# Optimization experiments

Hardware: AMD Instinct MI355X
Metric: run time of the kernel (lower is better)

The kernel has to match this reference:

```python
import jax, jax.numpy as jnp
import numpy as np

B, N, E, H = 2, 2048, 512, 8
D = E // H
SCALE_BASE = 512.0
EPS = 1e-6


def _xpos_tables(n, d):
    # XPOS (torchscale): per-dim scale ramp + standard sinusoidal freqs
    half = d // 2
    xscale = (np.arange(0, d, 2, dtype=np.float32) + 0.4 * d) / (1.4 * d)  # [half]
    min_pos = -(n // 2)
    power = (np.arange(min_pos, n + min_pos, dtype=np.float32) / SCALE_BASE)[:, None]
    scale = xscale[None, :] ** power                                       # [n, half]
    inv_freq = 1.0 / (10000.0 ** (np.arange(0, half, dtype=np.float32) / half))
    sinusoid = np.arange(n, dtype=np.float32)[:, None] * inv_freq[None, :]  # [n, half]
    return (jnp.asarray(np.sin(sinusoid), jnp.float32),
            jnp.asarray(np.cos(sinusoid), jnp.float32),
            jnp.asarray(scale, jnp.float32))


def _dup_interleave(m):
    # [n, half] -> [n, d], each column repeated twice interleaved
    return jnp.repeat(m, 2, axis=-1)


def _rotate_every_two(x):
    x1, x2 = x[..., ::2], x[..., 1::2]
    return jnp.stack((-x2, x1), axis=-1).reshape(x.shape)


def _apply_xpos(x, sin, cos, scale):
    s = _dup_interleave(sin * scale)  # [n, d]
    c = _dup_interleave(cos * scale)
    return x * c + _rotate_every_two(x) * s


def _decay_mask(n, dtype=jnp.float32):
    # gammas per head: 1 - exp(linspace(log(1/32), log(1/512), H))
    gammas = 1.0 - jnp.exp(jnp.linspace(np.log(1.0 / 32), np.log(1.0 / 512), H)).astype(dtype)
    pos = jnp.arange(n, dtype=dtype)
    dist = pos[:, None] - pos[None, :]                 # [n, s]
    dist_c = jnp.where(dist >= 0, dist, 0.0)
    return jnp.where(dist[None] >= 0, gammas[:, None, None] ** dist_c[None], 0.0)  # [h, n, s]


def _msr_forward(query, key, value, Wq, bq, Wk, bk, Wv, bv, Wg, bg, Wo, bo):
    b, n, e = query.shape
    q = (query @ Wq.T + bq).reshape(b, n, H, D).transpose(0, 2, 1, 3)  # [b,h,n,d]
    k = (key   @ Wk.T + bk).reshape(b, n, H, D).transpose(0, 2, 1, 3)
    v = (value @ Wv.T + bv).reshape(b, n, H, D).transpose(0, 2, 1, 3)

    sin, cos, scale = _xpos_tables(n, D)
    q = _apply_xpos(q, sin, cos, scale)
    k = _apply_xpos(k, sin, cos, 1.0 / scale)  # downscale=True

    k = k / jnp.asarray(np.sqrt(D), q.dtype)   # scale = head_dim ** 0.5
    mask = _decay_mask(n, q.dtype)             # [h,n,s]

    sim = jnp.einsum('bhnd,bhsd->bhns', q, k) * mask[None]
    ret = jnp.einsum('bhns,bhsd->bhnd', sim, v)  # [b,h,n,d]

    # GroupNorm(groups=H, channels=H, affine=False) on [(b n), h, d]:
    # normalize each (b, n, h) slice over its d elements
    mean = ret.mean(axis=-1, keepdims=True)
    var = ret.var(axis=-1, keepdims=True)
    ret = (ret - mean) / jnp.sqrt(var + EPS)

    ret = ret.transpose(0, 2, 1, 3).reshape(b, n, e)
    gate = jax.nn.silu(query @ Wg.T + bg)
    return (ret * gate) @ Wo.T + bo


def setup_inputs() -> dict:
    key = jax.random.key(0)
    ks = jax.random.split(key, 13)
    std = float(np.sqrt(2.0 / (E + E)))  # xavier_normal for square Linear
    mk = lambda k: jax.random.normal(k, (E, E), jnp.float32) * std
    return {
        'query': jax.random.normal(ks[0], (B, N, E), jnp.float32),
        'key':   jax.random.normal(ks[1], (B, N, E), jnp.float32),
        'value': jax.random.normal(ks[2], (B, N, E), jnp.float32),
        'Wq': mk(ks[3]), 'bq': jnp.zeros((E,), jnp.float32),
        'Wk': mk(ks[4]), 'bk': jnp.zeros((E,), jnp.float32),
        'Wv': mk(ks[5]), 'bv': jnp.zeros((E,), jnp.float32),
        'Wg': mk(ks[6]), 'bg': jnp.zeros((E,), jnp.float32),
        'Wo': mk(ks[7]), 'bo': jnp.zeros((E,), jnp.float32),
    }


def reference(query, key, value, Wq, bq, Wk, bk, Wv, bv, Wg, bg, Wo, bo):
    return _msr_forward(query, key, value, Wq, bq, Wk, bk, Wv, bv, Wg, bg, Wo, bo)
```

## Files before the change

### kernel.cpp

```cpp
#include <hip/hip_runtime.h>
#include <math.h>

#define Bc 2
#define Nc 2048
#define Ec 512
#define Hc 8
#define Dc 64
#define Mc 4096
#define NT 32
#define Cc 64

typedef short bf16x8 __attribute__((ext_vector_type(8)));
typedef float f32x4 __attribute__((ext_vector_type(4)));

#define GLOAD(g, l) __builtin_amdgcn_global_load_lds(                        \
    (const __attribute__((address_space(1))) unsigned*)(const void*)(g),     \
    (__attribute__((address_space(3))) unsigned*)(void*)(l), 16, 0, 0)

#define VMCNT(n) asm volatile("s_waitcnt vmcnt(" #n ")" ::: "memory")

__device__ __forceinline__ unsigned short f2bf(float x) {
    union { float f; unsigned u; } v; v.f = x;
    unsigned r = v.u + 0x7fffu + ((v.u >> 16) & 1u);
    return (unsigned short)(r >> 16);
}
__device__ __forceinline__ float bf2f(unsigned short b) {
    union { float f; unsigned u; } v; v.u = ((unsigned)b) << 16;
    return v.f;
}

__device__ __forceinline__ float get_gamma(int h) {
    const float l0 = -3.4657359028f;
    const float l1 = -6.2383246250f;
    return 1.0f - expf(l0 + (l1 - l0) * ((float)h / 7.0f));
}

struct SplitArgs {
    const float* src[8];
    unsigned short* hi[8];
    unsigned short* lo[8];
    int n[8];
};

__global__ __launch_bounds__(256) void prep_kernel(SplitArgs a,
                                                   float* __restrict__ sinS,
                                                   float* __restrict__ cosS,
                                                   float* __restrict__ sinIS,
                                                   float* __restrict__ cosIS) {
    int y = blockIdx.y;
    if (y == 8) {
        int idx = blockIdx.x * 256 + threadIdx.x;
        if (idx >= Nc * 32) return;
        int n = idx & 2047;
        int i = idx >> 11;
        float xscale = (2.0f * (float)i + 25.6f) / 89.6f;
        float power  = ((float)n - 1024.0f) / 512.0f;
        float scale  = powf(xscale, power);
        float inv_freq = powf(10000.0f, -(float)i / 32.0f);
        float ang = (float)n * inv_freq;
        float s = sinf(ang), c = cosf(ang);
        int o = i * 2048 + n;
        sinS[o]  = s * scale;
        cosS[o]  = c * scale;
        float rs = 0.125f / scale;
        sinIS[o] = s * rs;
        cosIS[o] = c * rs;
        return;
    }
    int i4 = (blockIdx.x * 256 + threadIdx.x) * 4;
    if (i4 >= a.n[y]) return;
    float4 v = *(const float4*)&a.src[y][i4];
    ushort4 h, l;
    h.x = f2bf(v.x); l.x = f2bf(v.x - bf2f(h.x));
    h.y = f2bf(v.y); l.y = f2bf(v.y - bf2f(h.y));
    h.z = f2bf(v.z); l.z = f2bf(v.z - bf2f(h.z));
    h.w = f2bf(v.w); l.w = f2bf(v.w - bf2f(h.w));
    *(ushort4*)&a.hi[y][i4] = h;
    *(ushort4*)&a.lo[y][i4] = l;
}

template<int TM, int TN, int WR, int WC>
__global__ __launch_bounds__(WR * WC * 64) void mgemm_kernel(
    const unsigned short* __restrict__ Xq_h, const unsigned short* __restrict__ Xq_l,
    const unsigned short* __restrict__ Xk_h, const unsigned short* __restrict__ Xk_l,
    const unsigned short* __restrict__ Xv_h, const unsigned short* __restrict__ Xv_l,
    const unsigned short* __restrict__ Xr_h, const unsigned short* __restrict__ Xr_l,
    const unsigned short* __restrict__ Wq_h, const unsigned short* __restrict__ Wq_l,
    const unsigned short* __restrict__ Wk_h, const unsigned short* __restrict__ Wk_l,
    const unsigned short* __restrict__ Wv_h, const unsigned short* __restrict__ Wv_l,
    const unsigned short* __restrict__ Wg_h, const unsigned short* __restrict__ Wg_l,
    const unsigned short* __restrict__ Wo_h, const unsigned short* __restrict__ Wo_l,
    const float* __restrict__ bq, const float* __restrict__ bk, const float* __restrict__ bv,
    const float* __restrict__ bg, const float* __restrict__ bo,
    float* __restrict__ Qr, float* __restrict__ Kr, float* __restrict__ Vr,
    float* __restrict__ G, float* __restrict__ Out,
    const float* __restrict__ sinS, const float* __restrict__ cosS,
    const float* __restrict__ sinIS, const float* __restrict__ cosIS,
    int mode_base)
{
    constexpr int THREADS = WR * WC * 64;
    constexpr int MI  = TM / WR / 16;
    constexpr int NI  = TN / WC / 16;
    constexpr int RA  = TM * 4 / THREADS;
    constexpr int RB  = TN * 4 / THREADS;
    constexpr int GL  = 2 * (RA + RB);
    constexpr int BUF = (TM + TN) * 64;
    constexpr int ALo = TM * 32;
    constexpr int BHo = TM * 64;
    constexpr int BLo = TM * 64 + TN * 32;
    static_assert(GL == 6 || GL == 8, "vmcnt literal");

    int gx = gridDim.x, gy = gridDim.y;
    int nwg = gx * gy * gridDim.z;
    int id = blockIdx.x + gx * (blockIdx.y + gy * blockIdx.z);
    int sid = (id & 7) * (nwg >> 3) + (id >> 3);
    int bx = sid % gx; int rest = sid / gx;
    int by = rest % gy; int bz = rest / gy;

    int mode = mode_base + bz;
    const unsigned short *Xh, *Xl, *Wh, *Wl; const float* bias;
    switch (mode) {
        case 0:  Xh = Xq_h; Xl = Xq_l; Wh = Wq_h; Wl = Wq_l; bias = bq; break;
        case 1:  Xh = Xk_h; Xl = Xk_l; Wh = Wk_h; Wl = Wk_l; bias = bk; break;
        case 2:  Xh = Xv_h; Xl = Xv_l; Wh = Wv_h; Wl = Wv_l; bias = bv; break;
        case 3:  Xh = Xq_h; Xl = Xq_l; Wh = Wg_h; Wl = Wg_l; bias = bg; break;
        default: Xh = Xr_h; Xl = Xr_l; Wh = Wo_h; Wl = Wo_l; bias = bo; break;
    }

    __shared__ __align__(16) short lds[2 * BUF];

    int tid  = threadIdx.x;
    int lane = tid & 63;
    int w    = tid >> 6;
    int wr   = w / WC, wc = w % WC;
    int row0 = bx * TM, col0 = by * TN;
    int lrow = lane & 15, lslot = lane >> 4;

    f32x4 acc[MI][NI];
    #pragma unroll
    for (int i = 0; i < MI; ++i)
        #pragma unroll
        for (int j = 0; j < NI; ++j) acc[i][j] = {0.f, 0.f, 0.f, 0.f};

    int aoff[MI], boff[NI];
    #pragma unroll
    for (int mi = 0; mi < MI; ++mi) {
        int r = wr * (TM / WR) + mi * 16 + lrow;
        aoff[mi] = (r * 4 + (lslot ^ ((r >> 1) & 3))) * 8;
    }
    #pragma unroll
    for (int ni = 0; ni < NI; ++ni) {
        int r = wc * (TN / WC) + ni * 16 + lrow;
        boff[ni] = (r * 4 + (lslot ^ ((r >> 1) & 3))) * 8;
    }

    auto stage = [&](int buf, int k0) {
        short* l = &lds[buf * BUF];
        #pragma unroll
        for (int i = 0; i < RA; ++i) {
            int q = i * THREADS + tid;
            int r = q >> 2;
            int sp = (q & 3) ^ ((r >> 1) & 3);
            int base = (i * THREADS + (w << 6)) * 8;
            size_t ga = (size_t)(row0 + r) * Ec + k0 + sp * 8;
            GLOAD(Xh + ga, &l[base]);
            GLOAD(Xl + ga, &l[ALo + base]);
        }
        #pragma unroll
        for (int i = 0; i < RB; ++i) {
            int q = i * THREADS + tid;
            int r = q >> 2;
            int sp = (q & 3) ^ ((r >> 1) & 3);
            int base = (i * THREADS + (w << 6)) * 8;
            size_t gb = (size_t)(col0 + r) * Ec + k0 + sp * 8;
            GLOAD(Wh + gb, &l[BHo + base]);
            GLOAD(Wl + gb, &l[BLo + base]);
        }
    };

    stage(0, 0);
    for (int t = 0; t < Ec / 32; ++t) {
        int cur = t & 1;
        if (t < Ec / 32 - 1) {
            stage(cur ^ 1, (t + 1) * 32);
            if constexpr (GL == 6) VMCNT(6); else VMCNT(8);
        } else {
            VMCNT(0);
        }
        __builtin_amdgcn_s_barrier();
        __builtin_amdgcn_sched_barrier(0);

        const short* l = &lds[cur * BUF];
        bf16x8 ah[MI], al[MI], bh[NI], bl[NI];
        #pragma unroll
        for (int mi = 0; mi < MI; ++mi) {
            ah[mi] = *(const bf16x8*)&l[aoff[mi]];
            al[mi] = *(const bf16x8*)&l[ALo + aoff[mi]];
        }
        #pragma unroll
        for (int ni = 0; ni < NI; ++ni) {
            bh[ni] = *(const bf16x8*)&l[BHo + boff[ni]];
            bl[ni] = *(const bf16x8*)&l[BLo + boff[ni]];
        }
        #pragma unroll
        for (int mi = 0; mi < MI; ++mi)
            #pragma unroll
            for (int ni = 0; ni < NI; ++ni) {
                acc[mi][ni] = __builtin_amdgcn_mfma_f32_16x16x32_bf16(ah[mi], bh[ni], acc[mi][ni], 0, 0, 0);
                acc[mi][ni] = __builtin_amdgcn_mfma_f32_16x16x32_bf16(ah[mi], bl[ni], acc[mi][ni], 0, 0, 0);
                acc[mi][ni] = __builtin_amdgcn_mfma_f32_16x16x32_bf16(al[mi], bh[ni], acc[mi][ni], 0, 0, 0);
            }
        asm volatile("s_waitcnt lgkmcnt(0)" ::: "memory");
        __builtin_amdgcn_sched_barrier(0);
        __builtin_amdgcn_s_barrier();
    }

    int quad = lslot;
    if (mode <= 1) {
        const float* st = (mode == 0) ? sinS : sinIS;
        const float* ct = (mode == 0) ? cosS : cosIS;
        float* dst = (mode == 0) ? Qr : Kr;
        #pragma unroll
        for (int ni = 0; ni < NI; ++ni) {
            int c = col0 + wc * (TN / WC) + ni * 16 + lrow;
            int h = c >> 6, d = c & 63, pr = d >> 1;
            float bi = bias[c];
            #pragma unroll
            for (int mi = 0; mi < MI; ++mi) {
                int R0 = row0 + wr * (TM / WR) + mi * 16 + quad * 4;
                int bb = R0 >> 11;
                int n0 = R0 & 2047;
                float4 sv4 = *(const float4*)&st[pr * 2048 + n0];
                float4 cv4 = *(const float4*)&ct[pr * 2048 + n0];
                float svv[4] = {sv4.x, sv4.y, sv4.z, sv4.w};
                float cvv[4] = {cv4.x, cv4.y, cv4.z, cv4.w};
                #pragma unroll
                for (int reg = 0; reg < 4; ++reg) {
                    float x = acc[mi][ni][reg] + bi;
                    float p = __shfl_xor(x, 1, 64);
                    float y = (c & 1) ? fmaf(x, cvv[reg],  p * svv[reg])
                                      : fmaf(x, cvv[reg], -p * svv[reg]);
                    dst[(((size_t)(bb * Hc + h)) * Nc + n0 + reg) * Dc + d] = y;
                }
            }
        }
    } else if (mode == 2) {
        #pragma unroll
        for (int ni = 0; ni < NI; ++ni) {
            int c = col0 + wc * (TN / WC) + ni * 16 + lrow;
            int h = c >> 6, d = c & 63;
            float bi = bias[c];
            #pragma unroll
            for (int mi = 0; mi < MI; ++mi) {
                int R0 = row0 + wr * (TM / WR) + mi * 16 + quad * 4;
                int bb = R0 >> 11;
                int n0 = R0 & 2047;
                #pragma unroll
                for (int reg = 0; reg < 4; ++reg)
                    Vr[(((size_t)(bb * Hc + h)) * Nc + n0 + reg) * Dc + d] =
                        acc[mi][ni][reg] + bi;
            }
        }
    } else {
        #pragma unroll
        for (int ni = 0; ni < NI; ++ni) {
            int c = col0 + wc * (TN / WC) + ni * 16 + lrow;
            float bi = bias[c];
            #pragma unroll
            for (int mi = 0; mi < MI; ++mi) {
                int R0 = row0 + wr * (TM / WR) + mi * 16 + quad * 4;
                #pragma unroll
                for (int reg = 0; reg < 4; ++reg) {
                    float x = acc[mi][ni][reg] + bi;
                    if (mode == 3)
                        G[(size_t)(R0 + reg) * Ec + c] = x / (1.0f + expf(-x));
                    else
                        Out[(size_t)(R0 + reg) * Ec + c] = x;
                }
            }
        }
    }
}

__global__ __launch_bounds__(256) void phaseA_kernel(const float* __restrict__ Kr,
                                                     const float* __restrict__ Vr,
                                                     float* __restrict__ L)
{
    int bh = blockIdx.x;
    int t  = blockIdx.y;
    float gamma = get_gamma(bh & 7);
    float lg = logf(gamma);

    __shared__ float Ks[64][68];
    __shared__ float Vs[64][68];

    int tid = threadIdx.x;
    const float* Kc = Kr + (size_t)(bh * Nc + t * Cc) * Dc;
    const float* Vc = Vr + (size_t)(bh * Nc + t * Cc) * Dc;

    #pragma unroll
    for (int i = 0; i < 4; ++i) {
        int f = tid + i * 256;
        int s = f >> 4;
        int d = (f & 15) << 2;
        float w = expf(lg * (float)(Cc - s));
        float4 kv = *(const float4*)&Kc[s * Dc + d];
        float4 ks = {kv.x * w, kv.y * w, kv.z * w, kv.w * w};
        *(float4*)&Ks[s][d] = ks;
        float4 vv = *(const float4*)&Vc[s * Dc + d];
        *(float4*)&Vs[s][d] = vv;
    }
    __syncthreads();

    int tx = tid & 15, ty = tid >> 4;
    float acc[4][4];
    #pragma unroll
    for (int i = 0; i < 4; ++i)
        #pragma unroll
        for (int j = 0; j < 4; ++j) acc[i][j] = 0.0f;

    for (int s = 0; s < 64; ++s) {
        float4 a = *(const float4*)&Ks[s][ty * 4];
        float4 b = *(const float4*)&Vs[s][tx * 4];
        float av[4] = {a.x, a.y, a.z, a.w};
        float bv[4] = {b.x, b.y, b.z, b.w};
        #pragma unroll
        for (int i = 0; i < 4; ++i)
            #pragma unroll
            for (int j = 0; j < 4; ++j)
                acc[i][j] = fmaf(av[i], bv[j], acc[i][j]);
    }

    float* Lp = L + (size_t)(bh * NT + t) * 4096;
    #pragma unroll
    for (int i = 0; i < 4; ++i) {
        float4 o = {acc[i][0], acc[i][1], acc[i][2], acc[i][3]};
        *(float4*)&Lp[(ty * 4 + i) * 64 + tx * 4] = o;
    }
}

__global__ __launch_bounds__(256) void scan_kernel(const float* __restrict__ L,
                                                   float* __restrict__ Sst)
{
    int bh = blockIdx.x;
    int part = blockIdx.y;
    int tid = threadIdx.x;
    float gamma = get_gamma(bh & 7);
    float g64 = expf(logf(gamma) * 64.0f);

    float4 s = {0.0f, 0.0f, 0.0f, 0.0f};
    size_t base = (size_t)bh * NT * 4096 + part * 1024 + tid * 4;
    const float* Lp = L + base;
    float* Sp = Sst + base;
    for (int t = 0; t < NT; ++t) {
        *(float4*)&Sp[(size_t)t * 4096] = s;
        float4 l = *(const float4*)&Lp[(size_t)t * 4096];
        s.x = s.x * g64 + l.x;
        s.y = s.y * g64 + l.y;
        s.z = s.z * g64 + l.z;
        s.w = s.w * g64 + l.w;
    }
}

__global__ __launch_bounds__(256) void phaseC_kernel(
    const float* __restrict__ Qr, const float* __restrict__ Kr, const float* __restrict__ Vr,
    const float* __restrict__ Sst, const float* __restrict__ G,
    unsigned short* __restrict__ retGh, unsigned short* __restrict__ retGl)
{
    int bh = blockIdx.x, t = blockIdx.y;
    int b = bh >> 3, h = bh & 7;
    float gamma = get_gamma(h);
    float lg = logf(gamma);

    __shared__ float QsT[64][68];
    __shared__ float KsT[64][68];
    __shared__ float Ss[64][68];

    int tid = threadIdx.x;
    const float* Qc = Qr + (size_t)(bh * Nc + t * Cc) * Dc;
    const float* Kc = Kr + (size_t)(bh * Nc + t * Cc) * Dc;
    const float* Sp = Sst + (size_t)(bh * NT + t) * 4096;

    #pragma unroll
    for (int i = 0; i < 4; ++i) {
        int f = tid + i * 256;
        int r = f >> 4;
        int d = (f & 15) << 2;
        float wq = expf(lg * (float)r);
        float4 q = *(const float4*)&Qc[r * Dc + d];
        QsT[d + 0][r] = q.x * wq; QsT[d + 1][r] = q.y * wq;
        QsT[d + 2][r] = q.z * wq; QsT[d + 3][r] = q.w * wq;
        float wk = expf(-lg * (float)r);
        float4 kk = *(const float4*)&Kc[r * Dc + d];
        KsT[d + 0][r] = kk.x * wk; KsT[d + 1][r] = kk.y * wk;
        KsT[d + 2][r] = kk.z * wk; KsT[d + 3][r] = kk.w * wk;
        float4 sv = *(const float4*)&Sp[r * 64 + d];
        *(float4*)&Ss[r][d] = sv;
    }
    __syncthreads();

    int tx = tid & 15, ty = tid >> 4;
    float accA[4][4], accO[4][4];
    #pragma unroll
    for (int i = 0; i < 4; ++i)
        #pragma unroll
        for (int j = 0; j < 4; ++j) { accA[i][j] = 0.0f; accO[i][j] = 0.0f; }

    for (int d = 0; d < 64; ++d) {
        float4 a  = *(const float4*)&QsT[d][ty * 4];
        float4 kb = *(const float4*)&KsT[d][tx * 4];
        float4 sb = *(const float4*)&Ss[d][tx * 4];
        float av[4] = {a.x, a.y, a.z, a.w};
        float kv[4] = {kb.x, kb.y, kb.z, kb.w};
        float sv[4] = {sb.x, sb.y, sb.z, sb.w};
        #pragma unroll
        for (int i = 0; i < 4; ++i)
            #pragma unroll
            for (int j = 0; j < 4; ++j) {
                accA[i][j] = fmaf(av[i], kv[j], accA[i][j]);
                accO[i][j] = fmaf(av[i], sv[j], accO[i][j]);
            }
    }
    __syncthreads();

    #pragma unroll
    for (int i = 0; i < 4; ++i) {
        int gi = ty * 4 + i;
        #pragma unroll
        for (int j = 0; j < 4; ++j) {
            int gj = tx * 4 + j;
            KsT[gj][gi] = (gj <= gi) ? accA[i][j] : 0.0f;
        }
    }
    const float* Vc = Vr + (size_t)(bh * Nc + t * Cc) * Dc;
    #pragma unroll
    for (int i = 0; i < 4; ++i) {
        int f = tid + i * 256;
        int r = f >> 4;
        int d = (f & 15) << 2;
        float4 vv = *(const float4*)&Vc[r * Dc + d];
        *(float4*)&QsT[r][d] = vv;
    }
    __syncthreads();

    for (int j = 0; j < 64; ++j) {
        float4 a = *(const float4*)&KsT[j][ty * 4];
        float4 v = *(const float4*)&QsT[j][tx * 4];
        float av[4] = {a.x, a.y, a.z, a.w};
        float vv[4] = {v.x, v.y, v.z, v.w};
        #pragma unroll
        for (int i = 0; i < 4; ++i)
            #pragma unroll
            for (int jj = 0; jj < 4; ++jj)
                accO[i][jj] = fmaf(av[i], vv[jj], accO[i][jj]);
    }

    #pragma unroll
    for (int i = 0; i < 4; ++i) {
        float sum = accO[i][0] + accO[i][1] + accO[i][2] + accO[i][3];
        float sq  = accO[i][0] * accO[i][0] + accO[i][1] * accO[i][1]
                  + accO[i][2] * accO[i][2] + accO[i][3] * accO[i][3];
        #pragma unroll
        for (int m = 1; m < 16; m <<= 1) {
            sum += __shfl_xor(sum, m, 64);
            sq  += __shfl_xor(sq,  m, 64);
        }
        float mean = sum * (1.0f / 64.0f);
        float var  = sq * (1.0f / 64.0f) - mean * mean;
        float rinv = rsqrtf(var + 1e-6f);
        #pragma unroll
        for (int jj = 0; jj < 4; ++jj)
            accO[i][jj] = (accO[i][jj] - mean) * rinv;
    }

    #pragma unroll
    for (int i = 0; i < 4; ++i) {
        int n = t * Cc + ty * 4 + i;
        size_t idx = ((size_t)b * Nc + n) * Ec + h * Dc + tx * 4;
        float4 g = *(const float4*)&G[idx];
        float o0 = accO[i][0] * g.x, o1 = accO[i][1] * g.y;
        float o2 = accO[i][2] * g.z, o3 = accO[i][3] * g.w;
        ushort4 hh, ll;
        hh.x = f2bf(o0); ll.x = f2bf(o0 - bf2f(hh.x));
        hh.y = f2bf(o1); ll.y = f2bf(o1 - bf2f(hh.y));
        hh.z = f2bf(o2); ll.z = f2bf(o2 - bf2f(hh.z));
        hh.w = f2bf(o3); ll.w = f2bf(o3 - bf2f(hh.w));
        *(ushort4*)&retGh[idx] = hh;
        *(ushort4*)&retGl[idx] = ll;
    }
}

extern "C" void kernel_launch(void* const* d_in, const int* in_sizes, int n_in,
                              void* d_out, int out_size, void* d_ws, size_t ws_size,
                              hipStream_t stream) {
    const float* query = (const float*)d_in[0];
    const float* key   = (const float*)d_in[1];
    const float* value = (const float*)d_in[2];
    const float* Wq = (const float*)d_in[3];
    const float* bq = (const float*)d_in[4];
    const float* Wk = (const float*)d_in[5];
    const float* bk = (const float*)d_in[6];
    const float* Wv = (const float*)d_in[7];
    const float* bv = (const float*)d_in[8];
    const float* Wg = (const float*)d_in[9];
    const float* bg = (const float*)d_in[10];
    const float* Wo = (const float*)d_in[11];
    const float* bo = (const float*)d_in[12];
    float* out = (float*)d_out;

    float* wsf = (float*)d_ws;
    const size_t SZ = (size_t)Bc * Nc * Ec;

    float* Qr = wsf;
    float* Kr = Qr + SZ;
    float* Vr = Kr + SZ;
    float* G  = Vr + SZ;

    unsigned short* Xq_h = (unsigned short*)(wsf + 4 * SZ);
    unsigned short* Xq_l = Xq_h + SZ;
    unsigned short* Xk_h = Xq_l + SZ;
    unsigned short* Xk_l = Xk_h + SZ;
    unsigned short* Xv_h = Xk_l + SZ;
    unsigned short* Xv_l = Xv_h + SZ;
    float* L   = wsf + 4 * SZ;
    float* Sst = wsf + 5 * SZ;
    unsigned short* retGh = (unsigned short*)(wsf + 6 * SZ);
    unsigned short* retGl = retGh + SZ;

    const size_t WSZ = (size_t)Ec * Ec;
    unsigned short* Wp = (unsigned short*)(wsf + 7 * SZ);
    unsigned short* Wq_h = Wp;            unsigned short* Wq_l = Wp + WSZ;
    unsigned short* Wk_h = Wp + 2 * WSZ;  unsigned short* Wk_l = Wp + 3 * WSZ;
    unsigned short* Wv_h = Wp + 4 * WSZ;  unsigned short* Wv_l = Wp + 5 * WSZ;
    unsigned short* Wg_h = Wp + 6 * WSZ;  unsigned short* Wg_l = Wp + 7 * WSZ;
    unsigned short* Wo_h = Wp + 8 * WSZ;  unsigned short* Wo_l = Wp + 9 * WSZ;

    float* tab = wsf + 7 * SZ + (10 * WSZ) / 2;
    float* sinS  = tab;
    float* cosS  = sinS + Nc * 32;
    float* sinIS = cosS + Nc * 32;
    float* cosIS = sinIS + Nc * 32;

    SplitArgs sa;
    sa.src[0] = query; sa.hi[0] = Xq_h; sa.lo[0] = Xq_l; sa.n[0] = (int)SZ;
    sa.src[1] = key;   sa.hi[1] = Xk_h; sa.lo[1] = Xk_l; sa.n[1] = (int)SZ;
    sa.src[2] = value; sa.hi[2] = Xv_h; sa.lo[2] = Xv_l; sa.n[2] = (int)SZ;
    sa.src[3] = Wq;    sa.hi[3] = Wq_h; sa.lo[3] = Wq_l; sa.n[3] = (int)WSZ;
    sa.src[4] = Wk;    sa.hi[4] = Wk_h; sa.lo[4] = Wk_l; sa.n[4] = (int)WSZ;
    sa.src[5] = Wv;    sa.hi[5] = Wv_h; sa.lo[5] = Wv_l; sa.n[5] = (int)WSZ;
    sa.src[6] = Wg;    sa.hi[6] = Wg_h; sa.lo[6] = Wg_l; sa.n[6] = (int)WSZ;
    sa.src[7] = Wo;    sa.hi[7] = Wo_h; sa.lo[7] = Wo_l; sa.n[7] = (int)WSZ;
    prep_kernel<<<dim3(2048, 9), dim3(256), 0, stream>>>(sa, sinS, cosS, sinIS, cosIS);

    mgemm_kernel<128, 256, 2, 4><<<dim3(Mc / 128, Ec / 256, 4), dim3(512), 0, stream>>>(
        Xq_h, Xq_l, Xk_h, Xk_l, Xv_h, Xv_l, retGh, retGl,
        Wq_h, Wq_l, Wk_h, Wk_l, Wv_h, Wv_l, Wg_h, Wg_l, Wo_h, Wo_l,
        bq, bk, bv, bg, bo, Qr, Kr, Vr, G, out,
        sinS, cosS, sinIS, cosIS, 0);

    phaseA_kernel<<<dim3(Bc * Hc, NT), dim3(256), 0, stream>>>(Kr, Vr, L);
    scan_kernel<<<dim3(Bc * Hc, 4), dim3(256), 0, stream>>>(L, Sst);
    phaseC_kernel<<<dim3(Bc * Hc, NT), dim3(256), 0, stream>>>(Qr, Kr, Vr, Sst, G, retGh, retGl);

    mgemm_kernel<128, 128, 2, 2><<<dim3(Mc / 128, Ec / 128, 1), dim3(256), 0, stream>>>(
        Xq_h, Xq_l, Xk_h, Xk_l, Xv_h, Xv_l, retGh, retGl,
        Wq_h, Wq_l, Wk_h, Wk_l, Wv_h, Wv_l, Wg_h, Wg_l, Wo_h, Wo_l,
        bq, bk, bv, bg, bo, Qr, Kr, Vr, G, out,
        sinS, cosS, sinIS, cosIS, 4);
}
```

Measured before the change: 189.1 us.

## Triple-buffer GEMM with load portions interleaved between MFMA phases

The double-buffered GEMM main loop becomes a triple-buffered one that prefetches two K-steps ahead. Each step is split into four phases, one per B column block. Each phase issues a slice of the next global-to-LDS loads, then runs its MFMAs at raised wave priority. The output-projection GEMM also moves to 64x128 tiles to launch more workgroups. The aim is to hide memory latency behind MFMA work, at the cost of more LDS per block and more barriers per K-step.

```diff
diff --git a/kernel.cpp b/kernel.cpp
--- a/kernel.cpp
+++ b/kernel.cpp
@@ -103,12 +103,12 @@
     constexpr int NI  = TN / WC / 16;
     constexpr int RA  = TM * 4 / THREADS;
     constexpr int RB  = TN * 4 / THREADS;
-    constexpr int GL  = 2 * (RA + RB);
     constexpr int BUF = (TM + TN) * 64;
     constexpr int ALo = TM * 32;
     constexpr int BHo = TM * 64;
     constexpr int BLo = TM * 64 + TN * 32;
-    static_assert(GL == 6 || GL == 8, "vmcnt literal");
+    constexpr int NSTEP = Ec / 32;
+    static_assert(RA == 1 && RB == 2 && NI == 4, "phase schedule assumes this shape");
 
     int gx = gridDim.x, gy = gridDim.y;
     int nwg = gx * gy * gridDim.z;
@@ -127,7 +127,7 @@
         default: Xh = Xr_h; Xl = Xr_l; Wh = Wo_h; Wl = Wo_l; bias = bo; break;
     }
 
-    __shared__ __align__(16) short lds[2 * BUF];
+    __shared__ __align__(16) short lds[3 * BUF];
 
     int tid  = threadIdx.x;
     int lane = tid & 63;
@@ -154,14 +154,13 @@
         boff[ni] = (r * 4 + (lslot ^ ((r >> 1) & 3))) * 8;
     }
 
-    auto stage = [&](int buf, int k0) {
+    auto stage_full = [&](int buf, int k0) {
         short* l = &lds[buf * BUF];
-        #pragma unroll
-        for (int i = 0; i < RA; ++i) {
-            int q = i * THREADS + tid;
+        {
+            int q = tid;
             int r = q >> 2;
             int sp = (q & 3) ^ ((r >> 1) & 3);
-            int base = (i * THREADS + (w << 6)) * 8;
+            int base = (w << 6) * 8;
             size_t ga = (size_t)(row0 + r) * Ec + k0 + sp * 8;
             GLOAD(Xh + ga, &l[base]);
             GLOAD(Xl + ga, &l[ALo + base]);
@@ -177,42 +176,66 @@
             GLOAD(Wl + gb, &l[BLo + base]);
         }
     };
-
-    stage(0, 0);
-    for (int t = 0; t < Ec / 32; ++t) {
-        int cur = t & 1;
-        if (t < Ec / 32 - 1) {
-            stage(cur ^ 1, (t + 1) * 32);
-            if constexpr (GL == 6) VMCNT(6); else VMCNT(8);
-        } else {
-            VMCNT(0);
-        }
-        __builtin_amdgcn_s_barrier();
-        __builtin_amdgcn_sched_barrier(0);
-
+    auto stage_portion = [&](int buf, int k0, int p) {
+        short* l = &lds[buf * BUF];
+        if (p == 0) {
+            int q = tid;
+            int r = q >> 2;
+            int sp = (q & 3) ^ ((r >> 1) & 3);
+            int base = (w << 6) * 8;
+            size_t ga = (size_t)(row0 + r) * Ec + k0 + sp * 8;
+            GLOAD(Xh + ga, &l[base]);
+            GLOAD(Xl + ga, &l[ALo + base]);
+        } else if (p <= 2) {
+            int i = p - 1;
+            int q = i * THREADS + tid;
+            int r = q >> 2;
+            int sp = (q & 3) ^ ((r >> 1) & 3);
+            int base = (i * THREADS + (w << 6)) * 8;
+            size_t gb = (size_t)(col0 + r) * Ec + k0 + sp * 8;
+            GLOAD(Wh + gb, &l[BHo + base]);
+            GLOAD(Wl + gb, &l[BLo + base]);
+        }
+    };
+
+    stage_full(0, 0);
+    stage_full(1, 32);
+    VMCNT(6);
+    __builtin_amdgcn_s_barrier();
+
+    bf16x8 ah[MI], al[MI];
+    for (int t = 0; t < NSTEP; ++t) {
+        const int cur = t % 3;
         const short* l = &lds[cur * BUF];
-        bf16x8 ah[MI], al[MI], bh[NI], bl[NI];
-        #pragma unroll
-        for (int mi = 0; mi < MI; ++mi) {
-            ah[mi] = *(const bf16x8*)&l[aoff[mi]];
-            al[mi] = *(const bf16x8*)&l[ALo + aoff[mi]];
-        }
-        #pragma unroll
-        for (int ni = 0; ni < NI; ++ni) {
-            bh[ni] = *(const bf16x8*)&l[BHo + boff[ni]];
-            bl[ni] = *(const bf16x8*)&l[BLo + boff[ni]];
-        }
-        #pragma unroll
-        for (int mi = 0; mi < MI; ++mi)
-            #pragma unroll
-            for (int ni = 0; ni < NI; ++ni) {
-                acc[mi][ni] = __builtin_amdgcn_mfma_f32_16x16x32_bf16(ah[mi], bh[ni], acc[mi][ni], 0, 0, 0);
-                acc[mi][ni] = __builtin_amdgcn_mfma_f32_16x16x32_bf16(ah[mi], bl[ni], acc[mi][ni], 0, 0, 0);
-                acc[mi][ni] = __builtin_amdgcn_mfma_f32_16x16x32_bf16(al[mi], bh[ni], acc[mi][ni], 0, 0, 0);
+        const bool pre = (t + 2) < NSTEP;
+        const int nb = (t + 2) % 3;
+        const int nk = (t + 2) * 32;
+        #pragma unroll
+        for (int p = 0; p < 4; ++p) {
+            if (p == 0) {
+                #pragma unroll
+                for (int mi = 0; mi < MI; ++mi) {
+                    ah[mi] = *(const bf16x8*)&l[aoff[mi]];
+                    al[mi] = *(const bf16x8*)&l[ALo + aoff[mi]];
+                }
             }
-        asm volatile("s_waitcnt lgkmcnt(0)" ::: "memory");
-        __builtin_amdgcn_sched_barrier(0);
-        __builtin_amdgcn_s_barrier();
+            bf16x8 bh2 = *(const bf16x8*)&l[BHo + boff[p]];
+            bf16x8 bl2 = *(const bf16x8*)&l[BLo + boff[p]];
+            if (pre) stage_portion(nb, nk, p);
+            __builtin_amdgcn_s_barrier();
+            asm volatile("s_waitcnt lgkmcnt(0)" ::: "memory");
+            __builtin_amdgcn_sched_barrier(0);
+            __builtin_amdgcn_s_setprio(1);
+            #pragma unroll
+            for (int mi = 0; mi < MI; ++mi) {
+                acc[mi][p] = __builtin_amdgcn_mfma_f32_16x16x32_bf16(ah[mi], bh2, acc[mi][p], 0, 0, 0);
+                acc[mi][p] = __builtin_amdgcn_mfma_f32_16x16x32_bf16(ah[mi], bl2, acc[mi][p], 0, 0, 0);
+                acc[mi][p] = __builtin_amdgcn_mfma_f32_16x16x32_bf16(al[mi], bh2, acc[mi][p], 0, 0, 0);
+            }
+            __builtin_amdgcn_s_setprio(0);
+            if (p == 3) { if (pre) VMCNT(6); else VMCNT(0); }
+            __builtin_amdgcn_s_barrier();
+        }
     }
 
     int quad = lslot;
@@ -237,9 +260,9 @@
                 #pragma unroll
                 for (int reg = 0; reg < 4; ++reg) {
                     float x = acc[mi][ni][reg] + bi;
-                    float p = __shfl_xor(x, 1, 64);
-                    float y = (c & 1) ? fmaf(x, cvv[reg],  p * svv[reg])
-                                      : fmaf(x, cvv[reg], -p * svv[reg]);
+                    float p2 = __shfl_xor(x, 1, 64);
+                    float y = (c & 1) ? fmaf(x, cvv[reg],  p2 * svv[reg])
+                                      : fmaf(x, cvv[reg], -p2 * svv[reg]);
                     dst[(((size_t)(bb * Hc + h)) * Nc + n0 + reg) * Dc + d] = y;
                 }
             }
@@ -562,7 +585,7 @@
     scan_kernel<<<dim3(Bc * Hc, 4), dim3(256), 0, stream>>>(L, Sst);
     phaseC_kernel<<<dim3(Bc * Hc, NT), dim3(256), 0, stream>>>(Qr, Kr, Vr, Sst, G, retGh, retGl);
 
-    mgemm_kernel<128, 128, 2, 2><<<dim3(Mc / 128, Ec / 128, 1), dim3(256), 0, stream>>>(
+    mgemm_kernel<64, 128, 2, 2><<<dim3(Mc / 64, Ec / 128, 1), dim3(256), 0, stream>>>(
         Xq_h, Xq_l, Xk_h, Xk_l, Xv_h, Xv_l, retGh, retGl,
         Wq_h, Wq_l, Wk_h, Wk_l, Wv_h, Wv_l, Wg_h, Wg_l, Wo_h, Wo_l,
         bq, bk, bv, bg, bo, Qr, Kr, Vr, G, out,
```

Measured after the change: 178.1 us. 1.06x faster.

## Replace split-bf16 three-pass GEMMs with single fp16 MFMA and retune tiles

Applied to the files above, without the earlier changes.

Replaces the hi/lo bf16 split representation (three MFMAs per tile pair plus double loads) with a single fp16 conversion and one f16 MFMA per tile, halving staging traffic and cutting matrix work by about three times. The GEMM tile shapes are also changed (the QKVG projection uses 128x128 with 256 threads, the output projection uses 64x128), and the scan kernel is regridded to more, smaller blocks. The epilogue is moved into a helper. The main risk is accuracy: fp16 has a narrower range and fewer mantissa bits than the compensated split, so the result may drift from the fp32 reference.

```diff
diff --git a/kernel.cpp b/kernel.cpp
--- a/kernel.cpp
+++ b/kernel.cpp
@@ -10,7 +10,7 @@
 #define NT 32
 #define Cc 64
 
-typedef short bf16x8 __attribute__((ext_vector_type(8)));
+typedef _Float16 f16x8 __attribute__((ext_vector_type(8)));
 typedef float f32x4 __attribute__((ext_vector_type(4)));
 
 #define GLOAD(g, l) __builtin_amdgcn_global_load_lds(                        \
@@ -19,15 +19,7 @@
 
 #define VMCNT(n) asm volatile("s_waitcnt vmcnt(" #n ")" ::: "memory")
 
-__device__ __forceinline__ unsigned short f2bf(float x) {
-    union { float f; unsigned u; } v; v.f = x;
-    unsigned r = v.u + 0x7fffu + ((v.u >> 16) & 1u);
-    return (unsigned short)(r >> 16);
-}
-__device__ __forceinline__ float bf2f(unsigned short b) {
-    union { float f; unsigned u; } v; v.u = ((unsigned)b) << 16;
-    return v.f;
-}
+union H4 { _Float16 h[4]; ushort4 u; };
 
 __device__ __forceinline__ float get_gamma(int h) {
     const float l0 = -3.4657359028f;
@@ -37,8 +29,7 @@
 
 struct SplitArgs {
     const float* src[8];
-    unsigned short* hi[8];
-    unsigned short* lo[8];
+    unsigned short* dst[8];
     int n[8];
 };
 
@@ -70,26 +61,94 @@
     int i4 = (blockIdx.x * 256 + threadIdx.x) * 4;
     if (i4 >= a.n[y]) return;
     float4 v = *(const float4*)&a.src[y][i4];
-    ushort4 h, l;
-    h.x = f2bf(v.x); l.x = f2bf(v.x - bf2f(h.x));
-    h.y = f2bf(v.y); l.y = f2bf(v.y - bf2f(h.y));
-    h.z = f2bf(v.z); l.z = f2bf(v.z - bf2f(h.z));
-    h.w = f2bf(v.w); l.w = f2bf(v.w - bf2f(h.w));
-    *(ushort4*)&a.hi[y][i4] = h;
-    *(ushort4*)&a.lo[y][i4] = l;
+    H4 o;
+    o.h[0] = (_Float16)v.x; o.h[1] = (_Float16)v.y;
+    o.h[2] = (_Float16)v.z; o.h[3] = (_Float16)v.w;
+    *(ushort4*)&a.dst[y][i4] = o.u;
+}
+
+template<int TM, int TN, int WR, int WC, int MI, int NI>
+__device__ __forceinline__ void gemm_epilogue(
+    f32x4 (&acc)[MI][NI], int mode, int row0, int col0, int wr, int wc,
+    int lrow, int quad, const float* bias,
+    float* Qr, float* Kr, float* Vr, float* G, float* Out,
+    unsigned short* retG,
+    const float* sinS, const float* cosS,
+    const float* sinIS, const float* cosIS)
+{
+    if (mode <= 1) {
+        const float* st = (mode == 0) ? sinS : sinIS;
+        const float* ct = (mode == 0) ? cosS : cosIS;
+        float* dst = (mode == 0) ? Qr : Kr;
+        #pragma unroll
+        for (int ni = 0; ni < NI; ++ni) {
+            int c = col0 + wc * (TN / WC) + ni * 16 + lrow;
+            int h = c >> 6, d = c & 63, pr = d >> 1;
+            float bi = bias[c];
+            #pragma unroll
+            for (int mi = 0; mi < MI; ++mi) {
+                int R0 = row0 + wr * (TM / WR) + mi * 16 + quad * 4;
+                int bb = R0 >> 11;
+                int n0 = R0 & 2047;
+                float4 sv4 = *(const float4*)&st[pr * 2048 + n0];
+                float4 cv4 = *(const float4*)&ct[pr * 2048 + n0];
+                float svv[4] = {sv4.x, sv4.y, sv4.z, sv4.w};
+                float cvv[4] = {cv4.x, cv4.y, cv4.z, cv4.w};
+                #pragma unroll
+                for (int reg = 0; reg < 4; ++reg) {
+                    float x = acc[mi][ni][reg] + bi;
+                    float p2 = __shfl_xor(x, 1, 64);
+                    float y = (c & 1) ? fmaf(x, cvv[reg],  p2 * svv[reg])
+                                      : fmaf(x, cvv[reg], -p2 * svv[reg]);
+                    dst[(((size_t)(bb * Hc + h)) * Nc + n0 + reg) * Dc + d] = y;
+                }
+            }
+        }
+    } else if (mode == 2) {
+        #pragma unroll
+        for (int ni = 0; ni < NI; ++ni) {
+            int c = col0 + wc * (TN / WC) + ni * 16 + lrow;
+            int h = c >> 6, d = c & 63;
+            float bi = bias[c];
+            #pragma unroll
+            for (int mi = 0; mi < MI; ++mi) {
+                int R0 = row0 + wr * (TM / WR) + mi * 16 + quad * 4;
+                int bb = R0 >> 11;
+                int n0 = R0 & 2047;
+                #pragma unroll
+                for (int reg = 0; reg < 4; ++reg)
+                    Vr[(((size_t)(bb * Hc + h)) * Nc + n0 + reg) * Dc + d] =
+                        acc[mi][ni][reg] + bi;
+            }
+        }
+    } else {
+        #pragma unroll
+        for (int ni = 0; ni < NI; ++ni) {
+            int c = col0 + wc * (TN / WC) + ni * 16 + lrow;
+            float bi = bias[c];
+            #pragma unroll
+            for (int mi = 0; mi < MI; ++mi) {
+                int R0 = row0 + wr * (TM / WR) + mi * 16 + quad * 4;
+                #pragma unroll
+                for (int reg = 0; reg < 4; ++reg) {
+                    float x = acc[mi][ni][reg] + bi;
+                    if (mode == 3)
+                        G[(size_t)(R0 + reg) * Ec + c] = x / (1.0f + expf(-x));
+                    else
+                        Out[(size_t)(R0 + reg) * Ec + c] = x;
+                }
+            }
+        }
+    }
 }
 
 template<int TM, int TN, int WR, int WC>
 __global__ __launch_bounds__(WR * WC * 64) void mgemm_kernel(
-    const unsigned short* __restrict__ Xq_h, const unsigned short* __restrict__ Xq_l,
-    const unsigned short* __restrict__ Xk_h, const unsigned short* __restrict__ Xk_l,
-    const unsigned short* __restrict__ Xv_h, const unsigned short* __restrict__ Xv_l,
-    const unsigned short* __restrict__ Xr_h, const unsigned short* __restrict__ Xr_l,
-    const unsigned short* __restrict__ Wq_h, const unsigned short* __restrict__ Wq_l,
-    const unsigned short* __restrict__ Wk_h, const unsigned short* __restrict__ Wk_l,
-    const unsigned short* __restrict__ Wv_h, const unsigned short* __restrict__ Wv_l,
-    const unsigned short* __restrict__ Wg_h, const unsigned short* __restrict__ Wg_l,
-    const unsigned short* __restrict__ Wo_h, const unsigned short* __restrict__ Wo_l,
+    const unsigned short* __restrict__ Xq, const unsigned short* __restrict__ Xk,
+    const unsigned short* __restrict__ Xv, const unsigned short* __restrict__ Xr,
+    const unsigned short* __restrict__ Wq, const unsigned short* __restrict__ Wk,
+    const unsigned short* __restrict__ Wv, const unsigned short* __restrict__ Wg,
+    const unsigned short* __restrict__ Wo,
     const float* __restrict__ bq, const float* __restrict__ bk, const float* __restrict__ bv,
     const float* __restrict__ bg, const float* __restrict__ bo,
     float* __restrict__ Qr, float* __restrict__ Kr, float* __restrict__ Vr,
@@ -103,12 +162,10 @@
     constexpr int NI  = TN / WC / 16;
     constexpr int RA  = TM * 4 / THREADS;
     constexpr int RB  = TN * 4 / THREADS;
-    constexpr int GL  = 2 * (RA + RB);
-    constexpr int BUF = (TM + TN) * 64;
-    constexpr int ALo = TM * 32;
-    constexpr int BHo = TM * 64;
-    constexpr int BLo = TM * 64 + TN * 32;
-    static_assert(GL == 6 || GL == 8, "vmcnt literal");
+    constexpr int GL  = RA + RB;
+    constexpr int BUF = (TM + TN) * 32;
+    constexpr int BHo = TM * 32;
+    static_assert(GL == 3 || GL == 4, "vmcnt literal");
 
     int gx = gridDim.x, gy = gridDim.y;
     int nwg = gx * gy * gridDim.z;
@@ -118,16 +175,16 @@
     int by = rest % gy; int bz = rest / gy;
 
     int mode = mode_base + bz;
-    const unsigned short *Xh, *Xl, *Wh, *Wl; const float* bias;
+    const unsigned short *Xh, *Wh; const float* bias;
     switch (mode) {
-        case 0:  Xh = Xq_h; Xl = Xq_l; Wh = Wq_h; Wl = Wq_l; bias = bq; break;
-        case 1:  Xh = Xk_h; Xl = Xk_l; Wh = Wk_h; Wl = Wk_l; bias = bk; break;
-        case 2:  Xh = Xv_h; Xl = Xv_l; Wh = Wv_h; Wl = Wv_l; bias = bv; break;
-        case 3:  Xh = Xq_h; Xl = Xq_l; Wh = Wg_h; Wl = Wg_l; bias = bg; break;
-        default: Xh = Xr_h; Xl = Xr_l; Wh = Wo_h; Wl = Wo_l; bias = bo; break;
-    }
-
-    __shared__ __align__(16) short lds[2 * BUF];
+        case 0:  Xh = Xq; Wh = Wq; bias = bq; break;
+        case 1:  Xh = Xk; Wh = Wk; bias = bk; break;
+        case 2:  Xh = Xv; Wh = Wv; bias = bv; break;
+        case 3:  Xh = Xq; Wh = Wg; bias = bg; break;
+        default: Xh = Xr; Wh = Wo; bias = bo; break;
+    }
+
+    __shared__ __align__(16) unsigned short lds[2 * BUF];
 
     int tid  = threadIdx.x;
     int lane = tid & 63;
@@ -155,7 +212,7 @@
     }
 
     auto stage = [&](int buf, int k0) {
-        short* l = &lds[buf * BUF];
+        unsigned short* l = &lds[buf * BUF];
         #pragma unroll
         for (int i = 0; i < RA; ++i) {
             int q = i * THREADS + tid;
@@ -164,7 +221,6 @@
             int base = (i * THREADS + (w << 6)) * 8;
             size_t ga = (size_t)(row0 + r) * Ec + k0 + sp * 8;
             GLOAD(Xh + ga, &l[base]);
-            GLOAD(Xl + ga, &l[ALo + base]);
         }
         #pragma unroll
         for (int i = 0; i < RB; ++i) {
@@ -174,7 +230,6 @@
             int base = (i * THREADS + (w << 6)) * 8;
             size_t gb = (size_t)(col0 + r) * Ec + k0 + sp * 8;
             GLOAD(Wh + gb, &l[BHo + base]);
-            GLOAD(Wl + gb, &l[BLo + base]);
         }
     };
 
@@ -183,103 +238,34 @@
         int cur = t & 1;
         if (t < Ec / 32 - 1) {
             stage(cur ^ 1, (t + 1) * 32);
-            if constexpr (GL == 6) VMCNT(6); else VMCNT(8);
+            if constexpr (GL == 4) VMCNT(4); else VMCNT(3);
         } else {
             VMCNT(0);
         }
         __builtin_amdgcn_s_barrier();
         __builtin_amdgcn_sched_barrier(0);
 
-        const short* l = &lds[cur * BUF];
-        bf16x8 ah[MI], al[MI], bh[NI], bl[NI];
-        #pragma unroll
-        for (int mi = 0; mi < MI; ++mi) {
-            ah[mi] = *(const bf16x8*)&l[aoff[mi]];
-            al[mi] = *(const bf16x8*)&l[ALo + aoff[mi]];
-        }
-        #pragma unroll
-        for (int ni = 0; ni < NI; ++ni) {
-            bh[ni] = *(const bf16x8*)&l[BHo + boff[ni]];
-            bl[ni] = *(const bf16x8*)&l[BLo + boff[ni]];
-        }
+        const unsigned short* l = &lds[cur * BUF];
+        f16x8 ah[MI], bh[NI];
         #pragma unroll
         for (int mi = 0; mi < MI; ++mi)
-            #pragma unroll
-            for (int ni = 0; ni < NI; ++ni) {
-                acc[mi][ni] = __builtin_amdgcn_mfma_f32_16x16x32_bf16(ah[mi], bh[ni], acc[mi][ni], 0, 0, 0);
-                acc[mi][ni] = __builtin_amdgcn_mfma_f32_16x16x32_bf16(ah[mi], bl[ni], acc[mi][ni], 0, 0, 0);
-                acc[mi][ni] = __builtin_amdgcn_mfma_f32_16x16x32_bf16(al[mi], bh[ni], acc[mi][ni], 0, 0, 0);
-            }
+            ah[mi] = *(const f16x8*)&l[aoff[mi]];
+        #pragma unroll
+        for (int ni = 0; ni < NI; ++ni)
+            bh[ni] = *(const f16x8*)&l[BHo + boff[ni]];
+        #pragma unroll
+        for (int mi = 0; mi < MI; ++mi)
+            #pragma unroll
+            for (int ni = 0; ni < NI; ++ni)
+                acc[mi][ni] = __builtin_amdgcn_mfma_f32_16x16x32_f16(ah[mi], bh[ni], acc[mi][ni], 0, 0, 0);
         asm volatile("s_waitcnt lgkmcnt(0)" ::: "memory");
         __builtin_amdgcn_sched_barrier(0);
         __builtin_amdgcn_s_barrier();
     }
 
-    int quad = lslot;
-    if (mode <= 1) {
-        const float* st = (mode == 0) ? sinS : sinIS;
-        const float* ct = (mode == 0) ? cosS : cosIS;
-        float* dst = (mode == 0) ? Qr : Kr;
-        #pragma unroll
-        for (int ni = 0; ni < NI; ++ni) {
-            int c = col0 + wc * (TN / WC) + ni * 16 + lrow;
-            int h = c >> 6, d = c & 63, pr = d >> 1;
-            float bi = bias[c];
-            #pragma unroll
-            for (int mi = 0; mi < MI; ++mi) {
-                int R0 = row0 + wr * (TM / WR) + mi * 16 + quad * 4;
-                int bb = R0 >> 11;
-                int n0 = R0 & 2047;
-                float4 sv4 = *(const float4*)&st[pr * 2048 + n0];
-                float4 cv4 = *(const float4*)&ct[pr * 2048 + n0];
-                float svv[4] = {sv4.x, sv4.y, sv4.z, sv4.w};
-                float cvv[4] = {cv4.x, cv4.y, cv4.z, cv4.w};
-                #pragma unroll
-                for (int reg = 0; reg < 4; ++reg) {
-                    float x = acc[mi][ni][reg] + bi;
-                    float p = __shfl_xor(x, 1, 64);
-                    float y = (c & 1) ? fmaf(x, cvv[reg],  p * svv[reg])
-                                      : fmaf(x, cvv[reg], -p * svv[reg]);
-                    dst[(((size_t)(bb * Hc + h)) * Nc + n0 + reg) * Dc + d] = y;
-                }
-            }
-        }
-    } else if (mode == 2) {
-        #pragma unroll
-        for (int ni = 0; ni < NI; ++ni) {
-            int c = col0 + wc * (TN / WC) + ni * 16 + lrow;
-            int h = c >> 6, d = c & 63;
-            float bi = bias[c];
-            #pragma unroll
-            for (int mi = 0; mi < MI; ++mi) {
-                int R0 = row0 + wr * (TM / WR) + mi * 16 + quad * 4;
-                int bb = R0 >> 11;
-                int n0 = R0 & 2047;
-                #pragma unroll
-                for (int reg = 0; reg < 4; ++reg)
-                    Vr[(((size_t)(bb * Hc + h)) * Nc + n0 + reg) * Dc + d] =
-                        acc[mi][ni][reg] + bi;
-            }
-        }
-    } else {
-        #pragma unroll
-        for (int ni = 0; ni < NI; ++ni) {
-            int c = col0 + wc * (TN / WC) + ni * 16 + lrow;
-            float bi = bias[c];
-            #pragma unroll
-            for (int mi = 0; mi < MI; ++mi) {
-                int R0 = row0 + wr * (TM / WR) + mi * 16 + quad * 4;
-                #pragma unroll
-                for (int reg = 0; reg < 4; ++reg) {
-                    float x = acc[mi][ni][reg] + bi;
-                    if (mode == 3)
-                        G[(size_t)(R0 + reg) * Ec + c] = x / (1.0f + expf(-x));
-                    else
-                        Out[(size_t)(R0 + reg) * Ec + c] = x;
-                }
-            }
-        }
-    }
+    gemm_epilogue<TM, TN, WR, WC, MI, NI>(acc, mode, row0, col0, wr, wc,
+        lrow, lslot, bias, Qr, Kr, Vr, G, Out, (unsigned short*)nullptr,
+        sinS, cosS, sinIS, cosIS);
 }
 
 __global__ __launch_bounds__(256) void phaseA_kernel(const float* __restrict__ Kr,
@@ -339,8 +325,8 @@
     }
 }
 
-__global__ __launch_bounds__(256) void scan_kernel(const float* __restrict__ L,
-                                                   float* __restrict__ Sst)
+__global__ __launch_bounds__(64) void scan_kernel(const float* __restrict__ L,
+                                                  float* __restrict__ Sst)
 {
     int bh = blockIdx.x;
     int part = blockIdx.y;
@@ -349,7 +335,7 @@
     float g64 = expf(logf(gamma) * 64.0f);
 
     float4 s = {0.0f, 0.0f, 0.0f, 0.0f};
-    size_t base = (size_t)bh * NT * 4096 + part * 1024 + tid * 4;
+    size_t base = (size_t)bh * NT * 4096 + part * 256 + tid * 4;
     const float* Lp = L + base;
     float* Sp = Sst + base;
     for (int t = 0; t < NT; ++t) {
@@ -365,7 +351,7 @@
 __global__ __launch_bounds__(256) void phaseC_kernel(
     const float* __restrict__ Qr, const float* __restrict__ Kr, const float* __restrict__ Vr,
     const float* __restrict__ Sst, const float* __restrict__ G,
-    unsigned short* __restrict__ retGh, unsigned short* __restrict__ retGl)
+    unsigned short* __restrict__ retG)
 {
     int bh = blockIdx.x, t = blockIdx.y;
     int b = bh >> 3, h = bh & 7;
@@ -478,15 +464,12 @@
         int n = t * Cc + ty * 4 + i;
         size_t idx = ((size_t)b * Nc + n) * Ec + h * Dc + tx * 4;
         float4 g = *(const float4*)&G[idx];
-        float o0 = accO[i][0] * g.x, o1 = accO[i][1] * g.y;
-        float o2 = accO[i][2] * g.z, o3 = accO[i][3] * g.w;
-        ushort4 hh, ll;
-        hh.x = f2bf(o0); ll.x = f2bf(o0 - bf2f(hh.x));
-        hh.y = f2bf(o1); ll.y = f2bf(o1 - bf2f(hh.y));
-        hh.z = f2bf(o2); ll.z = f2bf(o2 - bf2f(hh.z));
-        hh.w = f2bf(o3); ll.w = f2bf(o3 - bf2f(hh.w));
-        *(ushort4*)&retGh[idx] = hh;
-        *(ushort4*)&retGl[idx] = ll;
+        H4 o;
+        o.h[0] = (_Float16)(accO[i][0] * g.x);
+        o.h[1] = (_Float16)(accO[i][1] * g.y);
+        o.h[2] = (_Float16)(accO[i][2] * g.z);
+        o.h[3] = (_Float16)(accO[i][3] * g.w);
+        *(ushort4*)&retG[idx] = o.u;
     }
 }
 
@@ -516,55 +499,52 @@
     float* Vr = Kr + SZ;
     float* G  = Vr + SZ;
 
-    unsigned short* Xq_h = (unsigned short*)(wsf + 4 * SZ);
-    unsigned short* Xq_l = Xq_h + SZ;
-    unsigned short* Xk_h = Xq_l + SZ;
-    unsigned short* Xk_l = Xk_h + SZ;
-    unsigned short* Xv_h = Xk_l + SZ;
-    unsigned short* Xv_l = Xv_h + SZ;
-    float* L   = wsf + 4 * SZ;
-    float* Sst = wsf + 5 * SZ;
-    unsigned short* retGh = (unsigned short*)(wsf + 6 * SZ);
-    unsigned short* retGl = retGh + SZ;
+    unsigned short* Xq_f  = (unsigned short*)(wsf + 4 * SZ);
+    unsigned short* Xk_f  = Xq_f + SZ;
+    unsigned short* Xv_f  = Xk_f + SZ;
+    unsigned short* retGf = Xv_f + SZ;
+
+    float* L   = wsf + 6 * SZ;
+    float* Sst = wsf + 7 * SZ;
 
     const size_t WSZ = (size_t)Ec * Ec;
-    unsigned short* Wp = (unsigned short*)(wsf + 7 * SZ);
-    unsigned short* Wq_h = Wp;            unsigned short* Wq_l = Wp + WSZ;
-    unsigned short* Wk_h = Wp + 2 * WSZ;  unsigned short* Wk_l = Wp + 3 * WSZ;
-    unsigned short* Wv_h = Wp + 4 * WSZ;  unsigned short* Wv_l = Wp + 5 * WSZ;
-    unsigned short* Wg_h = Wp + 6 * WSZ;  unsigned short* Wg_l = Wp + 7 * WSZ;
-    unsigned short* Wo_h = Wp + 8 * WSZ;  unsigned short* Wo_l = Wp + 9 * WSZ;
-
-    float* tab = wsf + 7 * SZ + (10 * WSZ) / 2;
+    unsigned short* Wp = (unsigned short*)(wsf + 8 * SZ);
+    unsigned short* Wq_f = Wp;
+    unsigned short* Wk_f = Wp + WSZ;
+    unsigned short* Wv_f = Wp + 2 * WSZ;
+    unsigned short* Wg_f = Wp + 3 * WSZ;
+    unsigned short* Wo_f = Wp + 4 * WSZ;
+
+    float* tab = wsf + 8 * SZ + (5 * WSZ) / 2;
     float* sinS  = tab;
     float* cosS  = sinS + Nc * 32;
     float* sinIS = cosS + Nc * 32;
     float* cosIS = sinIS + Nc * 32;
 
     SplitArgs sa;
-    sa.src[0] = query; sa.hi[0] = Xq_h; sa.lo[0] = Xq_l; sa.n[0] = (int)SZ;
-    sa.src[1] = key;   sa.hi[1] = Xk_h; sa.lo[1] = Xk_l; sa.n[1] = (int)SZ;
-    sa.src[2] = value; sa.hi[2] = Xv_h; sa.lo[2] = Xv_l; sa.n[2] = (int)SZ;
-    sa.src[3] = Wq;    sa.hi[3] = Wq_h; sa.lo[3] = Wq_l; sa.n[3] = (int)WSZ;
-    sa.src[4] = Wk;    sa.hi[4] = Wk_h; sa.lo[4] = Wk_l; sa.n[4] = (int)WSZ;
-    sa.src[5] = Wv;    sa.hi[5] = Wv_h; sa.lo[5] = Wv_l; sa.n[5] = (int)WSZ;
-    sa.src[6] = Wg;    sa.hi[6] = Wg_h; sa.lo[6] = Wg_l; sa.n[6] = (int)WSZ;
-    sa.src[7] = Wo;    sa.hi[7] = Wo_h; sa.lo[7] = Wo_l; sa.n[7] = (int)WSZ;
+    sa.src[0] = query; sa.dst[0] = Xq_f; sa.n[0] = (int)SZ;
+    sa.src[1] = key;   sa.dst[1] = Xk_f; sa.n[1] = (int)SZ;
+    sa.src[2] = value; sa.dst[2] = Xv_f; sa.n[2] = (int)SZ;
+    sa.src[3] = Wq;    sa.dst[3] = Wq_f; sa.n[3] = (int)WSZ;
+    sa.src[4] = Wk;    sa.dst[4] = Wk_f; sa.n[4] = (int)WSZ;
+    sa.src[5] = Wv;    sa.dst[5] = Wv_f; sa.n[5] = (int)WSZ;
+    sa.src[6] = Wg;    sa.dst[6] = Wg_f; sa.n[6] = (int)WSZ;
+    sa.src[7] = Wo;    sa.dst[7] = Wo_f; sa.n[7] = (int)WSZ;
     prep_kernel<<<dim3(2048, 9), dim3(256), 0, stream>>>(sa, sinS, cosS, sinIS, cosIS);
 
-    mgemm_kernel<128, 256, 2, 4><<<dim3(Mc / 128, Ec / 256, 4), dim3(512), 0, stream>>>(
-        Xq_h, Xq_l, Xk_h, Xk_l, Xv_h, Xv_l, retGh, retGl,
-        Wq_h, Wq_l, Wk_h, Wk_l, Wv_h, Wv_l, Wg_h, Wg_l, Wo_h, Wo_l,
+    mgemm_kernel<128, 128, 2, 2><<<dim3(Mc / 128, Ec / 128, 4), dim3(256), 0, stream>>>(
+        Xq_f, Xk_f, Xv_f, retGf,
+        Wq_f, Wk_f, Wv_f, Wg_f, Wo_f,
         bq, bk, bv, bg, bo, Qr, Kr, Vr, G, out,
         sinS, cosS, sinIS, cosIS, 0);
 
     phaseA_kernel<<<dim3(Bc * Hc, NT), dim3(256), 0, stream>>>(Kr, Vr, L);
-    scan_kernel<<<dim3(Bc * Hc, 4), dim3(256), 0, stream>>>(L, Sst);
-    phaseC_kernel<<<dim3(Bc * Hc, NT), dim3(256), 0, stream>>>(Qr, Kr, Vr, Sst, G, retGh, retGl);
-
-    mgemm_kernel<128, 128, 2, 2><<<dim3(Mc / 128, Ec / 128, 1), dim3(256), 0, stream>>>(
-        Xq_h, Xq_l, Xk_h, Xk_l, Xv_h, Xv_l, retGh, retGl,
-        Wq_h, Wq_l, Wk_h, Wk_l, Wv_h, Wv_l, Wg_h, Wg_l, Wo_h, Wo_l,
+    scan_kernel<<<dim3(Bc * Hc, 16), dim3(64), 0, stream>>>(L, Sst);
+    phaseC_kernel<<<dim3(Bc * Hc, NT), dim3(256), 0, stream>>>(Qr, Kr, Vr, Sst, G, retGf);
+
+    mgemm_kernel<64, 128, 2, 2><<<dim3(Mc / 64, Ec / 128, 1), dim3(256), 0, stream>>>(
+        Xq_f, Xk_f, Xv_f, retGf,
+        Wq_f, Wk_f, Wv_f, Wg_f, Wo_f,
         bq, bk, bv, bg, bo, Qr, Kr, Vr, G, out,
         sinS, cosS, sinIS, cosIS, 4);
 }
```

Measured after the change: 159.8 us. 1.18x faster.
